# Kernel optimization log

Measured on AMD Instinct MI355X. Metric: run time of the kernel, lower is better.

Reference implementation:

```python
import jax, jax.numpy as jnp
import numpy as np

C, W = 144, 77          # channel_count, batch_width
KW = 10                 # kernel_width
FC = 64                 # fc_segment_length
CONV_OUT = W - KW + 1   # 68
H2 = 128

def setup_inputs() -> dict:
    key = jax.random.key(0)
    ks = jax.random.split(key, 10)
    s_fc = 1.0 / np.sqrt(W)
    s2 = 1.0 / np.sqrt(C * FC + CONV_OUT)
    s3 = 1.0 / np.sqrt(H2)
    s_cv = 1.0 / np.sqrt(C * KW)
    return {
        "x": jax.random.normal(ks[0], (C, W), dtype=jnp.float32),
        "fc_w": jax.random.uniform(ks[1], (C, FC, W), minval=-s_fc, maxval=s_fc, dtype=jnp.float32),
        "fc_b": jax.random.uniform(ks[2], (C, FC), minval=-s_fc, maxval=s_fc, dtype=jnp.float32),
        "conv_w": jax.random.uniform(ks[3], (1, 1, C, KW), minval=-s_cv, maxval=s_cv, dtype=jnp.float32),
        "conv_b": jax.random.uniform(ks[4], (1,), minval=-s_cv, maxval=s_cv, dtype=jnp.float32),
        "w2": jax.random.uniform(ks[5], (H2, C * FC + CONV_OUT), minval=-s2, maxval=s2, dtype=jnp.float32),
        "b2": jax.random.uniform(ks[6], (H2,), minval=-s2, maxval=s2, dtype=jnp.float32),
        "w3": jax.random.uniform(ks[7], (1, H2), minval=-s3, maxval=s3, dtype=jnp.float32),
        "b3": jax.random.uniform(ks[8], (1,), minval=-s3, maxval=s3, dtype=jnp.float32),
    }

def reference(x, fc_w, fc_b, conv_w, conv_b, w2, b2, w3, b3):
    # 144 per-channel Linear(77,64) fused into one batched GEMV: [C,FC,W] @ [C,W] -> [C,FC]
    fc_out = jnp.einsum('cdw,cw->cd', fc_w, x) + fc_b   # [C, FC]
    fc_out = fc_out.reshape(-1)                          # [C*FC]
    # Conv2d(1,1,(C,KW),stride=1) over full-height input -> [CONV_OUT]
    conv = jax.lax.conv_general_dilated(
        x[None, None, :, :], conv_w,
        window_strides=(1, 1), padding='VALID',
        dimension_numbers=('NCHW', 'OIHW', 'NCHW'))     # [1,1,1,CONV_OUT]
    conv = conv.reshape(-1) + conv_b[0]                  # [CONV_OUT]
    concat = jnp.concatenate([fc_out, conv])             # [C*FC + CONV_OUT]
    h = jax.nn.relu(concat @ w2.T + b2)                  # [H2]
    out = jax.nn.relu(h @ w3.T + b3)                     # [1]
    return jax.nn.sigmoid(out)
```

## Files before the change

### kernel.cpp

```cpp
#include <hip/hip_runtime.h>
#include <math.h>

#define CC 144
#define WW 77
#define KW 10
#define FC 64
#define CONV_OUT 68
#define H2 128
#define CONCAT (CC*FC + CONV_OUT)
#define NBLK (CC + 1)

__global__ __launch_bounds__(256, 1) void partials_kernel(
    const float* __restrict__ x,
    const float* __restrict__ fc_w,
    const float* __restrict__ fc_b,
    const float* __restrict__ conv_w,
    const float* __restrict__ conv_b,
    const float* __restrict__ w2,
    float* __restrict__ partial)
{
    __shared__ float xs[WW];
    __shared__ float vals[CONV_OUT];
    __shared__ float xfull[CC*WW];
    __shared__ float cw[CC*KW];

    const int t = threadIdx.x;
    const int blk = blockIdx.x;

    if (blk < CC) {
        const int c = blk;
        if (t < WW) xs[t] = x[c*WW + t];
        __syncthreads();
        {
            const int d = t >> 2, p = t & 3;
            const float* wrow = fc_w + (size_t)(c*FC + d)*WW;
            float s = 0.f;
            for (int w = p; w < WW; w += 4) s += wrow[w] * xs[w];
            s += __shfl_down(s, 2, 4);
            s += __shfl_down(s, 1, 4);
            if (p == 0) vals[d] = s + fc_b[c*FC + d];
        }
        __syncthreads();
        if (t < H2) {
            const float* wrow = w2 + (size_t)t*CONCAT + c*FC;
            float s = 0.f;
            #pragma unroll
            for (int d = 0; d < FC; ++d) s += wrow[d] * vals[d];
            partial[(size_t)blk*H2 + t] = s;
        }
    } else {
        for (int i = t; i < CC*WW; i += 256) xfull[i] = x[i];
        for (int i = t; i < CC*KW; i += 256) cw[i] = conv_w[i];
        __syncthreads();
        if (t < CONV_OUT*2) {
            const int j = t >> 1, p = t & 1;
            float s = 0.f;
            for (int c = p; c < CC; c += 2) {
                const float* xr = xfull + c*WW + j;
                const float* wr = cw + c*KW;
                #pragma unroll
                for (int k = 0; k < KW; ++k) s += xr[k] * wr[k];
            }
            s += __shfl_down(s, 1, 2);
            if (p == 0) vals[j] = s + conv_b[0];
        }
        __syncthreads();
        if (t < H2) {
            const float* wrow = w2 + (size_t)t*CONCAT + CC*FC;
            float s = 0.f;
            #pragma unroll
            for (int j = 0; j < CONV_OUT; ++j) s += wrow[j] * vals[j];
            partial[(size_t)blk*H2 + t] = s;
        }
    }
}

__global__ __launch_bounds__(128, 1) void finale_kernel(
    const float* __restrict__ partial,
    const float* __restrict__ b2,
    const float* __restrict__ w3,
    const float* __restrict__ b3,
    float* __restrict__ out)
{
    __shared__ float red[2];
    const int t = threadIdx.x;

    float s = b2[t];
    for (int b = 0; b < NBLK; ++b)
        s += partial[(size_t)b*H2 + t];
    s = fmaxf(s, 0.f);
    float v = s * w3[t];

    #pragma unroll
    for (int off = 32; off > 0; off >>= 1) v += __shfl_down(v, off, 64);
    if ((t & 63) == 0) red[t >> 6] = v;
    __syncthreads();
    if (t == 0) {
        float r = fmaxf(red[0] + red[1] + b3[0], 0.f);
        out[0] = 1.0f / (1.0f + expf(-r));
    }
}

extern "C" void kernel_launch(void* const* d_in, const int* in_sizes, int n_in,
                              void* d_out, int out_size, void* d_ws, size_t ws_size,
                              hipStream_t stream) {
    const float* x      = (const float*)d_in[0];
    const float* fc_w   = (const float*)d_in[1];
    const float* fc_b   = (const float*)d_in[2];
    const float* conv_w = (const float*)d_in[3];
    const float* conv_b = (const float*)d_in[4];
    const float* w2     = (const float*)d_in[5];
    const float* b2     = (const float*)d_in[6];
    const float* w3     = (const float*)d_in[7];
    const float* b3     = (const float*)d_in[8];
    float* out = (float*)d_out;

    float* partial = (float*)d_ws;

    partials_kernel<<<NBLK, 256, 0, stream>>>(
        x, fc_w, fc_b, conv_w, conv_b, w2, partial);
    finale_kernel<<<1, 128, 0, stream>>>(partial, b2, w3, b3, out);
}
```

Before: 93.82 us.

## Fuse final reduction into partials kernel via last-block atomic counter

Merges the two-kernel pipeline into one launch. The last block to arrive, detected with an atomic counter, performs the final bias, ReLU, dot and sigmoid, which removes the second kernel launch and its dependency gap. Each block also prefetches its w2 slice into registers as float4 loads before the fc GEMV, so those loads overlap with the fc_w reads. The conv work is split across two blocks, and all 256 threads now share the w2 dot product. The counter is never reset; it relies on the workspace starting at a known poison value and on modulo arithmetic across calls, which is fragile.

```diff
diff --git a/kernel.cpp b/kernel.cpp
--- a/kernel.cpp
+++ b/kernel.cpp
@@ -8,96 +8,119 @@
 #define CONV_OUT 68
 #define H2 128
 #define CONCAT (CC*FC + CONV_OUT)
-#define NBLK (CC + 1)
+#define NCONVBLK 2
+#define NBLK (CC + NCONVBLK)
+#define POISON 0xAAAAAAAAu
 
-__global__ __launch_bounds__(256, 1) void partials_kernel(
+__global__ __launch_bounds__(256, 1) void fused_kernel(
     const float* __restrict__ x,
     const float* __restrict__ fc_w,
     const float* __restrict__ fc_b,
     const float* __restrict__ conv_w,
     const float* __restrict__ conv_b,
     const float* __restrict__ w2,
-    float* __restrict__ partial)
+    const float* __restrict__ b2,
+    const float* __restrict__ w3,
+    const float* __restrict__ b3,
+    float* __restrict__ out,
+    float* __restrict__ partial,
+    unsigned int* __restrict__ counter)
 {
-    __shared__ float xs[WW];
+    __shared__ float xpart[(CC/NCONVBLK)*WW];
+    __shared__ float cwp[(CC/NCONVBLK)*KW];
     __shared__ float vals[CONV_OUT];
-    __shared__ float xfull[CC*WW];
-    __shared__ float cw[CC*KW];
+    __shared__ float red[4];
+    __shared__ unsigned int last_flag;
 
     const int t = threadIdx.x;
     const int blk = blockIdx.x;
+    const int j = t >> 1, p = t & 1;
 
     if (blk < CC) {
         const int c = blk;
-        if (t < WW) xs[t] = x[c*WW + t];
+        float4 wreg[8];
+        const float4* wv = (const float4*)(w2 + (size_t)j*CONCAT + c*FC + p*32);
+        #pragma unroll
+        for (int i = 0; i < 8; ++i) wreg[i] = wv[i];
+
+        {
+            const int d = t >> 2, p4 = t & 3;
+            const float* wrow = fc_w + (size_t)(c*FC + d)*WW;
+            const float* xr = x + c*WW;
+            float s = 0.f;
+            for (int w = p4; w < WW; w += 4) s += wrow[w] * xr[w];
+            s += __shfl_down(s, 2, 4);
+            s += __shfl_down(s, 1, 4);
+            if (p4 == 0) vals[d] = s + fc_b[c*FC + d];
+        }
         __syncthreads();
         {
-            const int d = t >> 2, p = t & 3;
-            const float* wrow = fc_w + (size_t)(c*FC + d)*WW;
-            float s = 0.f;
-            for (int w = p; w < WW; w += 4) s += wrow[w] * xs[w];
-            s += __shfl_down(s, 2, 4);
-            s += __shfl_down(s, 1, 4);
-            if (p == 0) vals[d] = s + fc_b[c*FC + d];
-        }
-        __syncthreads();
-        if (t < H2) {
-            const float* wrow = w2 + (size_t)t*CONCAT + c*FC;
+            const float* vp = vals + p*32;
             float s = 0.f;
             #pragma unroll
-            for (int d = 0; d < FC; ++d) s += wrow[d] * vals[d];
-            partial[(size_t)blk*H2 + t] = s;
+            for (int i = 0; i < 8; ++i) {
+                float4 w4 = wreg[i];
+                s += w4.x*vp[4*i] + w4.y*vp[4*i+1] + w4.z*vp[4*i+2] + w4.w*vp[4*i+3];
+            }
+            s += __shfl_down(s, 1, 2);
+            if (p == 0) partial[(size_t)blk*H2 + j] = s;
         }
     } else {
-        for (int i = t; i < CC*WW; i += 256) xfull[i] = x[i];
-        for (int i = t; i < CC*KW; i += 256) cw[i] = conv_w[i];
+        const int cidx = blk - CC;
+        const int c0 = cidx * (CC/NCONVBLK);
+        const int NCH = CC/NCONVBLK;
+        for (int i = t; i < NCH*WW; i += 256) xpart[i] = x[c0*WW + i];
+        for (int i = t; i < NCH*KW; i += 256) cwp[i] = conv_w[c0*KW + i];
         __syncthreads();
         if (t < CONV_OUT*2) {
-            const int j = t >> 1, p = t & 1;
+            const int jj = t >> 1, pc = t & 1;
             float s = 0.f;
-            for (int c = p; c < CC; c += 2) {
-                const float* xr = xfull + c*WW + j;
-                const float* wr = cw + c*KW;
+            for (int ci = pc; ci < NCH; ci += 2) {
+                const float* xr = xpart + ci*WW + jj;
+                const float* wr = cwp + ci*KW;
                 #pragma unroll
                 for (int k = 0; k < KW; ++k) s += xr[k] * wr[k];
             }
             s += __shfl_down(s, 1, 2);
-            if (p == 0) vals[j] = s + conv_b[0];
+            if (pc == 0) vals[jj] = s + (cidx == 0 ? conv_b[0] : 0.f);
         }
         __syncthreads();
-        if (t < H2) {
-            const float* wrow = w2 + (size_t)t*CONCAT + CC*FC;
+        {
+            const float* vp = vals + p*34;
+            const float* wrow = w2 + (size_t)j*CONCAT + CC*FC + p*34;
             float s = 0.f;
             #pragma unroll
-            for (int j = 0; j < CONV_OUT; ++j) s += wrow[j] * vals[j];
-            partial[(size_t)blk*H2 + t] = s;
+            for (int i = 0; i < 34; ++i) s += wrow[i] * vp[i];
+            s += __shfl_down(s, 1, 2);
+            if (p == 0) partial[(size_t)blk*H2 + j] = s;
         }
     }
-}
 
-__global__ __launch_bounds__(128, 1) void finale_kernel(
-    const float* __restrict__ partial,
-    const float* __restrict__ b2,
-    const float* __restrict__ w3,
-    const float* __restrict__ b3,
-    float* __restrict__ out)
-{
-    __shared__ float red[2];
-    const int t = threadIdx.x;
-
-    float s = b2[t];
-    for (int b = 0; b < NBLK; ++b)
-        s += partial[(size_t)b*H2 + t];
-    s = fmaxf(s, 0.f);
-    float v = s * w3[t];
-
-    #pragma unroll
-    for (int off = 32; off > 0; off >>= 1) v += __shfl_down(v, off, 64);
-    if ((t & 63) == 0) red[t >> 6] = v;
+    __threadfence();
     __syncthreads();
     if (t == 0) {
-        float r = fmaxf(red[0] + red[1] + b3[0], 0.f);
-        out[0] = 1.0f / (1.0f + expf(-r));
+        unsigned int old = atomicAdd(counter, 1u);
+        last_flag = ((old - POISON) % (unsigned)NBLK == (unsigned)(NBLK - 1)) ? 1u : 0u;
+    }
+    __syncthreads();
+
+    if (last_flag) {
+        __threadfence();
+        float s = (p == 0) ? b2[j] : 0.f;
+        for (int b = p; b < NBLK; b += 2)
+            s += __hip_atomic_load(partial + (size_t)b*H2 + j,
+                                   __ATOMIC_RELAXED, __HIP_MEMORY_SCOPE_AGENT);
+        s += __shfl_down(s, 1, 2);
+        float v = 0.f;
+        if (p == 0) v = fmaxf(s, 0.f) * w3[j];
+        #pragma unroll
+        for (int off = 32; off > 0; off >>= 1) v += __shfl_down(v, off, 64);
+        if ((t & 63) == 0) red[t >> 6] = v;
+        __syncthreads();
+        if (t == 0) {
+            float r = fmaxf(red[0] + red[1] + red[2] + red[3] + b3[0], 0.f);
+            out[0] = 1.0f / (1.0f + expf(-r));
+        }
     }
 }
 
@@ -116,8 +139,9 @@
     float* out = (float*)d_out;
 
     float* partial = (float*)d_ws;
+    unsigned int* counter =
+        (unsigned int*)((char*)d_ws + (size_t)NBLK*H2*sizeof(float));
 
-    partials_kernel<<<NBLK, 256, 0, stream>>>(
-        x, fc_w, fc_b, conv_w, conv_b, w2, partial);
-    finale_kernel<<<1, 128, 0, stream>>>(partial, b2, w3, b3, out);
+    fused_kernel<<<NBLK, 256, 0, stream>>>(
+        x, fc_w, fc_b, conv_w, conv_b, w2, b2, w3, b3, out, partial, counter);
 }
```

Measured after the change: 107.7 us. 14.9% more time.
